# Performance work log

Measured on AMD Instinct MI355X. Metric: run time of the kernel, lower is better.

The kernel has to match this reference:

```python
import jax, jax.numpy as jnp
import numpy as np
from jax import lax

V = 32000   # vocab_size (len(word2id)+1)
I = 512     # txt_input_size (embedding dim / LSTM input)
H = 1024    # txt_hidden_size
IMG = 2048  # img_input_size == img_hidden_size (hidden_fc input)
B = 64      # batch
T = 64      # target length (decode runs T-1 steps)


def setup_inputs() -> dict:
    key = jax.random.key(0)
    ks = jax.random.split(key, 16)
    n = lambda k, shape, s=0.02: jax.random.normal(k, shape, jnp.float32) * s
    embed = n(ks[0], (V, I)).at[0].set(0.0)  # padding_idx=0 row is zero
    return {
        "src": jax.random.normal(ks[1], (B, IMG), jnp.float32),
        "tgt_ids": jax.random.randint(ks[2], (B, T), 0, V),
        "embed": embed,
        "W_h": n(ks[3], (H, IMG)), "b_h": jnp.zeros((H,), jnp.float32),
        "W_c": n(ks[4], (H, IMG)), "b_c": jnp.zeros((H,), jnp.float32),
        "W_ih": n(ks[5], (4 * H, I)), "W_hh": n(ks[6], (4 * H, H)),
        "b_ih": jnp.zeros((4 * H,), jnp.float32),
        "b_hh": jnp.zeros((4 * H,), jnp.float32),
        "W_out": n(ks[7], (V, H)), "b_out": jnp.zeros((V,), jnp.float32),
    }


def reference(src, tgt_ids, embed, W_h, b_h, W_c, b_c,
              W_ih, W_hh, b_ih, b_hh, W_out, b_out):
    # init_hidden: tanh(Linear(src)) for both hidden and cell
    h0 = jnp.tanh(src @ W_h.T + b_h)  # [B, H]
    c0 = jnp.tanh(src @ W_c.T + b_c)  # [B, H]

    x = embed[tgt_ids]                 # [B, T, I]
    xs = jnp.swapaxes(x[:, :-1, :], 0, 1)  # [T-1, B, I] teacher-forced inputs

    def step(carry, xt):
        h, c = carry
        g = xt @ W_ih.T + b_ih + h @ W_hh.T + b_hh  # [B, 4H], gate order i,f,g,o
        i, f, gg, o = jnp.split(g, 4, axis=-1)
        c = jax.nn.sigmoid(f) * c + jax.nn.sigmoid(i) * jnp.tanh(gg)
        h = jax.nn.sigmoid(o) * jnp.tanh(c)
        return (h, c), h

    _, hs = lax.scan(step, (h0, c0), xs)        # [T-1, B, H]
    outs = jnp.swapaxes(hs, 0, 1)               # [B, T-1, H]
    # dropout is identity in eval / deterministic reference
    logits = jnp.einsum('bth,vh->btv', outs, W_out) + b_out  # [B, T-1, V]
    logp = jax.nn.log_softmax(logits, axis=-1)

    tgt = tgt_ids[:, 1:]                        # [B, T-1]
    tok_lp = jnp.take_along_axis(logp, tgt[..., None], axis=2)[..., 0]
    mask = (tgt != 0)
    num_words = mask.sum()
    loss = -(tok_lp * mask).sum() / jnp.maximum(num_words, 1).astype(jnp.float32)
    return loss, num_words
```

## Files before the change

kernel.cpp:

```cpp
#include <hip/hip_runtime.h>
#include <math.h>

static constexpr int BB = 64;
static constexpr int TT = 64;
static constexpr int VV = 32000;
static constexpr int II = 512;
static constexpr int HH = 1024;
static constexpr int GG = 2048;
static constexpr int NT = 63;
static constexpr int NR = NT * BB;
static constexpr int MP = 4096;
static constexpr int NVB = 500;
static constexpr int VBS = 512;

using s16x8 = __attribute__((ext_vector_type(8))) short;
using f32x4 = __attribute__((ext_vector_type(4))) float;

__device__ __forceinline__ unsigned short f2bf(float f) {
    union { float f; unsigned u; } v; v.f = f;
    unsigned r = v.u + 0x7FFFu + ((v.u >> 16) & 1u);
    return (unsigned short)(r >> 16);
}
__device__ __forceinline__ float bf2f(unsigned short h) {
    union { unsigned u; float f; } v; v.u = ((unsigned)h) << 16;
    return v.f;
}

__device__ __forceinline__ void gload_lds16(const unsigned short* g,
                                            unsigned short* l) {
    __builtin_amdgcn_global_load_lds(
        (const __attribute__((address_space(1))) void*)g,
        (__attribute__((address_space(3))) void*)l, 16, 0, 0);
}

__global__ void cvt_kernel(const float* __restrict__ in,
                           unsigned short* __restrict__ out, int n4) {
    int idx = blockIdx.x * blockDim.x + threadIdx.x;
    int stride = gridDim.x * blockDim.x;
    for (int i = idx; i < n4; i += stride) {
        float4 v = ((const float4*)in)[i];
        ushort4 o;
        o.x = f2bf(v.x); o.y = f2bf(v.y); o.z = f2bf(v.z); o.w = f2bf(v.w);
        ((ushort4*)out)[i] = o;
    }
}

__global__ void gather_kernel(const float* __restrict__ embed,
                              const int* __restrict__ tgt_ids,
                              unsigned short* __restrict__ X,
                              int* __restrict__ TGT) {
    int idx = blockIdx.x * 256 + threadIdx.x;
    if (idx >= NR * (II / 4)) return;
    int r = idx / (II / 4);
    int kq = idx % (II / 4);
    int t = r / BB, b = r % BB;
    int tok = tgt_ids[b * TT + t];
    float4 v = ((const float4*)(embed + (size_t)tok * II))[kq];
    ushort4 o;
    o.x = f2bf(v.x); o.y = f2bf(v.y); o.z = f2bf(v.z); o.w = f2bf(v.w);
    ((ushort4*)(X + (size_t)r * II))[kq] = o;
    if (kq == 0) TGT[r] = tgt_ids[b * TT + t + 1];
}

__global__ __launch_bounds__(256) void init_hc_kernel(
    const float* __restrict__ src,
    const float* __restrict__ W_h, const float* __restrict__ b_h,
    const float* __restrict__ W_c, const float* __restrict__ b_c,
    unsigned short* __restrict__ HS, float* __restrict__ C) {
    int wave = blockIdx.x * 4 + (threadIdx.x >> 6);
    int lane = threadIdx.x & 63;
    int sel = wave >> 13;
    int rem = wave & 8191;
    int j = rem >> 3;
    int b0 = (rem & 7) * 8;
    const float* w = (sel ? W_c : W_h) + (size_t)j * GG;
    float acc[8] = {0.f,0.f,0.f,0.f,0.f,0.f,0.f,0.f};
    for (int k = lane; k < GG; k += 64) {
        float wv = w[k];
#pragma unroll
        for (int bb = 0; bb < 8; ++bb)
            acc[bb] += wv * src[(size_t)(b0 + bb) * GG + k];
    }
#pragma unroll
    for (int bb = 0; bb < 8; ++bb)
        for (int off = 32; off; off >>= 1)
            acc[bb] += __shfl_xor(acc[bb], off);
    if (lane == 0) {
        float bias = sel ? b_c[j] : b_h[j];
#pragma unroll
        for (int bb = 0; bb < 8; ++bb) {
            float v = tanhf(acc[bb] + bias);
            if (sel == 0) HS[(size_t)(b0 + bb) * HH + j] = f2bf(v);
            else          C[(size_t)(b0 + bb) * HH + j] = v;
        }
    }
}

template<int KTOT>
__device__ __forceinline__ void gemm_body(
    const unsigned short* __restrict__ Abase,
    const unsigned short* __restrict__ Bbase,
    unsigned short* Al, unsigned short* Bl,
    int tid, f32x4 (&acc)[4][4]) {
    int wv = tid >> 6, lane = tid & 63;
    int rl = lane & 15, lg = lane >> 4;
    int wr = wv >> 1, wc = wv & 1;
    int sw = rl & 7;
    for (int kc = 0; kc < KTOT; kc += 64) {
        if (kc) __syncthreads();
#pragma unroll
        for (int it = 0; it < 4; ++it) {
            int c = it * 256 + tid;
            int row = c >> 3, slot = c & 7;
            int sslot = slot ^ (row & 7);
            gload_lds16(Abase + (size_t)row * KTOT + kc + sslot * 8,
                        Al + (size_t)c * 8);
            gload_lds16(Bbase + (size_t)row * KTOT + kc + sslot * 8,
                        Bl + (size_t)c * 8);
        }
        __syncthreads();
#pragma unroll
        for (int ks = 0; ks < 2; ++ks) {
            int soff = ((ks * 4 + lg) ^ sw) * 8;
            s16x8 a[4], b[4];
#pragma unroll
            for (int mf = 0; mf < 4; ++mf)
                a[mf] = *(const s16x8*)&Al[(wr * 64 + mf * 16 + rl) * 64 + soff];
#pragma unroll
            for (int nf = 0; nf < 4; ++nf)
                b[nf] = *(const s16x8*)&Bl[(wc * 64 + nf * 16 + rl) * 64 + soff];
#pragma unroll
            for (int mf = 0; mf < 4; ++mf)
#pragma unroll
                for (int nf = 0; nf < 4; ++nf)
                    acc[mf][nf] = __builtin_amdgcn_mfma_f32_16x16x32_bf16(
                        a[mf], b[nf], acc[mf][nf], 0, 0, 0);
        }
    }
}

__global__ __launch_bounds__(256) void gx_kernel(
    const unsigned short* __restrict__ X,
    const unsigned short* __restrict__ Wih,
    const float* __restrict__ b_ih, const float* __restrict__ b_hh,
    unsigned short* __restrict__ Gx) {
    __shared__ unsigned short Al[128 * 64];
    __shared__ unsigned short Bl[128 * 64];
    int tid = threadIdx.x;
    int mblk = blockIdx.x, nblk = blockIdx.y;
    int rbase = mblk * 128, v0 = nblk * 128;
    f32x4 acc[4][4];
#pragma unroll
    for (int mf = 0; mf < 4; ++mf)
#pragma unroll
        for (int nf = 0; nf < 4; ++nf) acc[mf][nf] = (f32x4){0.f,0.f,0.f,0.f};
    gemm_body<II>(X + (size_t)rbase * II, Wih + (size_t)v0 * II, Al, Bl, tid, acc);
    int wv = tid >> 6, lane = tid & 63;
    int rl = lane & 15, lg = lane >> 4;
    int wr = wv >> 1, wc = wv & 1;
    float bsum[4];
#pragma unroll
    for (int nf = 0; nf < 4; ++nf) {
        int col = v0 + wc * 64 + nf * 16 + rl;
        bsum[nf] = b_ih[col] + b_hh[col];
    }
#pragma unroll
    for (int mf = 0; mf < 4; ++mf)
#pragma unroll
        for (int q = 0; q < 4; ++q) {
            int r = rbase + wr * 64 + mf * 16 + lg * 4 + q;
#pragma unroll
            for (int nf = 0; nf < 4; ++nf) {
                int col = v0 + wc * 64 + nf * 16 + rl;
                Gx[(size_t)r * 4096 + col] = f2bf(acc[mf][nf][q] + bsum[nf]);
            }
        }
}

__global__ __launch_bounds__(256) void lstm_step_kernel(
    unsigned short* __restrict__ HS,
    const unsigned short* __restrict__ Gx,
    const unsigned short* __restrict__ Whh,
    float* __restrict__ C, int t) {
    __shared__ float R[64 * 16];
    int tid = threadIdx.x;
    int wv = tid >> 6, lane = tid & 63;
    int rl = lane & 15, lg = lane >> 4;
    int u0 = blockIdx.x * 4;
    int grow = tid >> 2, gul = tid & 3;
    int gu = u0 + gul;
    const unsigned short* gx = Gx + (size_t)(t * BB + grow) * 4096 + gu;
    unsigned short gx0 = gx[0 * HH], gx1 = gx[1 * HH];
    unsigned short gx2 = gx[2 * HH], gx3 = gx[3 * HH];
    float cold = C[(size_t)grow * HH + gu];
    const unsigned short* h = HS + (size_t)t * (BB * HH);
    const unsigned short* Ab = h + (size_t)(wv * 16 + rl) * HH + lg * 8;
    int gate = rl >> 2, ul = rl & 3;
    const unsigned short* Bb = Whh + (size_t)(gate * HH + u0 + ul) * HH + lg * 8;
    f32x4 acc0 = {0.f,0.f,0.f,0.f}, acc1 = {0.f,0.f,0.f,0.f};
#pragma unroll
    for (int kc = 0; kc < HH; kc += 64) {
        s16x8 a0 = *(const s16x8*)(Ab + kc);
        s16x8 b0 = *(const s16x8*)(Bb + kc);
        acc0 = __builtin_amdgcn_mfma_f32_16x16x32_bf16(a0, b0, acc0, 0, 0, 0);
        s16x8 a1 = *(const s16x8*)(Ab + kc + 32);
        s16x8 b1 = *(const s16x8*)(Bb + kc + 32);
        acc1 = __builtin_amdgcn_mfma_f32_16x16x32_bf16(a1, b1, acc1, 0, 0, 0);
    }
    f32x4 acc = acc0 + acc1;
#pragma unroll
    for (int q = 0; q < 4; ++q) R[(wv * 16 + lg * 4 + q) * 16 + rl] = acc[q];
    __syncthreads();
    float iv = R[grow * 16 + 0 * 4 + gul] + bf2f(gx0);
    float fv = R[grow * 16 + 1 * 4 + gul] + bf2f(gx1);
    float gv = R[grow * 16 + 2 * 4 + gul] + bf2f(gx2);
    float ov = R[grow * 16 + 3 * 4 + gul] + bf2f(gx3);
    float si = 1.f / (1.f + __expf(-iv));
    float sf = 1.f / (1.f + __expf(-fv));
    float so = 1.f / (1.f + __expf(-ov));
    float cnew = sf * cold + si * tanhf(gv);
    float hv = so * tanhf(cnew);
    C[(size_t)grow * HH + gu] = cnew;
    HS[(size_t)(t + 1) * (BB * HH) + (size_t)grow * HH + gu] = f2bf(hv);
}

__global__ __launch_bounds__(256) void logits_kernel(
    const unsigned short* __restrict__ A,
    const unsigned short* __restrict__ Wo,
    const float* __restrict__ b_out,
    const int* __restrict__ TGT,
    float* __restrict__ PM, float* __restrict__ PS,
    float* __restrict__ TLOG) {
    __shared__ unsigned short Al[128 * 64];
    __shared__ unsigned short Bl[128 * 64];
    int tid = threadIdx.x;
    int mblk = blockIdx.x, nblk = blockIdx.y;
    int rbase = mblk * 128, v0 = nblk * 128;
    f32x4 acc[4][4];
#pragma unroll
    for (int mf = 0; mf < 4; ++mf)
#pragma unroll
        for (int nf = 0; nf < 4; ++nf) acc[mf][nf] = (f32x4){0.f,0.f,0.f,0.f};
    gemm_body<HH>(A + (size_t)rbase * HH, Wo + (size_t)v0 * HH, Al, Bl, tid, acc);
    int wv = tid >> 6, lane = tid & 63;
    int rl = lane & 15, lg = lane >> 4;
    int wr = wv >> 1, wc = wv & 1;
    int cb = v0 + wc * 64;
    float bo[4];
#pragma unroll
    for (int nf = 0; nf < 4; ++nf) bo[nf] = b_out[cb + nf * 16 + rl];
    int vb = nblk * 2 + wc;
#pragma unroll
    for (int mf = 0; mf < 4; ++mf) {
        int rb = rbase + wr * 64 + mf * 16 + lg * 4;
#pragma unroll
        for (int q = 0; q < 4; ++q) {
            int r = rb + q;
            int tg = TGT[r];
            float e[4];
            float m = -1e30f;
#pragma unroll
            for (int nf = 0; nf < 4; ++nf) {
                e[nf] = acc[mf][nf][q] + bo[nf];
                if (cb + nf * 16 + rl == tg) TLOG[r] = e[nf];
                m = fmaxf(m, e[nf]);
            }
#pragma unroll
            for (int msk = 1; msk < 16; msk <<= 1) m = fmaxf(m, __shfl_xor(m, msk));
            float s = 0.f;
#pragma unroll
            for (int nf = 0; nf < 4; ++nf) s += __expf(e[nf] - m);
#pragma unroll
            for (int msk = 1; msk < 16; msk <<= 1) s += __shfl_xor(s, msk);
            if (rl == 0) {
                PM[(size_t)r * VBS + vb] = m;
                PS[(size_t)r * VBS + vb] = s;
            }
        }
    }
}

__global__ void rowred_kernel(const float* __restrict__ PM,
                              const float* __restrict__ PS,
                              const float* __restrict__ TLOG,
                              const int* __restrict__ TGT,
                              float* __restrict__ ROWLP) {
    int r = blockIdx.x * 4 + (threadIdx.x >> 6);
    int lane = threadIdx.x & 63;
    if (r >= NR) return;
    const float* pm = PM + (size_t)r * VBS;
    const float* ps = PS + (size_t)r * VBS;
    float m = -1e30f;
    for (int vb = lane; vb < NVB; vb += 64) m = fmaxf(m, pm[vb]);
    for (int off = 32; off; off >>= 1) m = fmaxf(m, __shfl_xor(m, off));
    float s = 0.f;
    for (int vb = lane; vb < NVB; vb += 64) s += ps[vb] * __expf(pm[vb] - m);
    for (int off = 32; off; off >>= 1) s += __shfl_xor(s, off);
    if (lane == 0) {
        float lse = m + logf(s);
        float lp = TLOG[r] - lse;
        ROWLP[r] = (TGT[r] != 0) ? lp : 0.f;
    }
}

__global__ void final_kernel(const float* __restrict__ ROWLP,
                             const int* __restrict__ TGT,
                             float* __restrict__ out) {
    int tid = threadIdx.x;
    float sum = 0.f; int cnt = 0;
    for (int r = tid; r < NR; r += 256) {
        sum += ROWLP[r];
        cnt += (TGT[r] != 0);
    }
    for (int off = 32; off; off >>= 1) {
        sum += __shfl_xor(sum, off);
        cnt += __shfl_xor(cnt, off);
    }
    __shared__ float wsum[4];
    __shared__ int wcnt[4];
    if ((tid & 63) == 0) { wsum[tid >> 6] = sum; wcnt[tid >> 6] = cnt; }
    __syncthreads();
    if (tid == 0) {
        float S = wsum[0] + wsum[1] + wsum[2] + wsum[3];
        int Cc = wcnt[0] + wcnt[1] + wcnt[2] + wcnt[3];
        out[0] = -S / fmaxf((float)Cc, 1.f);
        out[1] = (float)Cc;
    }
}

extern "C" void kernel_launch(void* const* d_in, const int* in_sizes, int n_in,
                              void* d_out, int out_size, void* d_ws, size_t ws_size,
                              hipStream_t stream) {
    const float* src    = (const float*)d_in[0];
    const int*   tgtids = (const int*)d_in[1];
    const float* embed  = (const float*)d_in[2];
    const float* W_h    = (const float*)d_in[3];
    const float* b_h    = (const float*)d_in[4];
    const float* W_c    = (const float*)d_in[5];
    const float* b_c    = (const float*)d_in[6];
    const float* W_ih   = (const float*)d_in[7];
    const float* W_hh   = (const float*)d_in[8];
    const float* b_ih   = (const float*)d_in[9];
    const float* b_hh   = (const float*)d_in[10];
    const float* W_out  = (const float*)d_in[11];
    const float* b_out  = (const float*)d_in[12];
    float* out = (float*)d_out;

    char* ws = (char*)d_ws;
    size_t off = 0;
    auto alloc = [&](size_t bytes) {
        size_t cur = off;
        off += (bytes + 255) & ~(size_t)255;
        return cur;
    };
    unsigned short* Wo_bf  = (unsigned short*)(ws + alloc((size_t)VV * HH * 2));
    unsigned short* Whh_bf = (unsigned short*)(ws + alloc((size_t)4 * HH * HH * 2));
    unsigned short* Wih_bf = (unsigned short*)(ws + alloc((size_t)4 * HH * II * 2));
    unsigned short* X_bf   = (unsigned short*)(ws + alloc((size_t)MP * II * 2));
    unsigned short* HS     = (unsigned short*)(ws + alloc((size_t)65 * BB * HH * 2));
    float* Cst   = (float*)(ws + alloc((size_t)BB * HH * 4));
    unsigned short* Gx = (unsigned short*)(ws + alloc((size_t)MP * 4096 * 2));
    float* PM    = (float*)(ws + alloc((size_t)MP * VBS * 4));
    float* PS    = (float*)(ws + alloc((size_t)MP * VBS * 4));
    float* TLOG  = (float*)(ws + alloc((size_t)MP * 4));
    int*   TGT   = (int*)(ws + alloc((size_t)MP * 4));
    float* ROWLP = (float*)(ws + alloc((size_t)NR * 4));

    cvt_kernel<<<4096, 256, 0, stream>>>(W_out, Wo_bf, VV * HH / 4);
    cvt_kernel<<<1024, 256, 0, stream>>>(W_hh, Whh_bf, 4 * HH * HH / 4);
    cvt_kernel<<<512, 256, 0, stream>>>(W_ih, Wih_bf, 4 * HH * II / 4);
    gather_kernel<<<(NR * (II / 4) + 255) / 256, 256, 0, stream>>>(embed, tgtids, X_bf, TGT);
    init_hc_kernel<<<4096, 256, 0, stream>>>(src, W_h, b_h, W_c, b_c, HS, Cst);
    gx_kernel<<<dim3(MP / 128, 4096 / 128), 256, 0, stream>>>(
        X_bf, Wih_bf, b_ih, b_hh, Gx);
    for (int t = 0; t < NT; ++t) {
        lstm_step_kernel<<<256, 256, 0, stream>>>(HS, Gx, Whh_bf, Cst, t);
    }
    logits_kernel<<<dim3(MP / 128, VV / 128), 256, 0, stream>>>(
        HS + (size_t)BB * HH, Wo_bf, b_out, TGT, PM, PS, TLOG);
    rowred_kernel<<<NR / 4, 256, 0, stream>>>(PM, PS, TLOG, TGT, ROWLP);
    final_kernel<<<1, 256, 0, stream>>>(ROWLP, TGT, out);
}
```

Before: 1.087 ms.

## Stage W_hh slice in LDS and widen LSTM step blocks to 16 units

Each LSTM step block now handles 16 hidden units with 1024 threads. It first stages the corresponding 64 rows of W_hh into padded shared memory, and 16 waves share the h reads and the staged weights. The goal is to stop re-fetching the hidden state from global memory by many small blocks and to reuse weights across the four M tiles. In exchange, only 64 blocks launch per step, leaving most CUs idle, and each step pays an LDS staging phase plus a barrier.

```diff
diff --git a/kernel.cpp b/kernel.cpp
--- a/kernel.cpp
+++ b/kernel.cpp
@@ -177,26 +177,37 @@
         }
 }
 
-__global__ __launch_bounds__(256) void lstm_step_kernel(
+static constexpr int BSTR = 1032;
+__global__ __launch_bounds__(1024, 1) void lstm_step_kernel(
     unsigned short* __restrict__ HS,
     const unsigned short* __restrict__ Gx,
     const unsigned short* __restrict__ Whh,
     float* __restrict__ C, int t) {
-    __shared__ float R[64 * 16];
+    __shared__ unsigned short Bs[64 * BSTR];
+    __shared__ float R[64 * 68];
     int tid = threadIdx.x;
-    int wv = tid >> 6, lane = tid & 63;
-    int rl = lane & 15, lg = lane >> 4;
-    int u0 = blockIdx.x * 4;
-    int grow = tid >> 2, gul = tid & 3;
+    int u0 = blockIdx.x * 16;
+    int grow = tid >> 4, gul = tid & 15;
     int gu = u0 + gul;
     const unsigned short* gx = Gx + (size_t)(t * BB + grow) * 4096 + gu;
     unsigned short gx0 = gx[0 * HH], gx1 = gx[1 * HH];
     unsigned short gx2 = gx[2 * HH], gx3 = gx[3 * HH];
     float cold = C[(size_t)grow * HH + gu];
-    const unsigned short* h = HS + (size_t)t * (BB * HH);
-    const unsigned short* Ab = h + (size_t)(wv * 16 + rl) * HH + lg * 8;
-    int gate = rl >> 2, ul = rl & 3;
-    const unsigned short* Bb = Whh + (size_t)(gate * HH + u0 + ul) * HH + lg * 8;
+#pragma unroll
+    for (int it = 0; it < 8; ++it) {
+        int id = it * 1024 + tid;
+        int br = id >> 7, k8 = (id & 127) * 8;
+        int ul = br >> 2, g = br & 3;
+        *(uint4*)&Bs[br * BSTR + k8] =
+            *(const uint4*)(Whh + (size_t)(g * HH + u0 + ul) * HH + k8);
+    }
+    __syncthreads();
+    int wv = tid >> 6, lane = tid & 63;
+    int mt = wv >> 2, nt = wv & 3;
+    int rl = lane & 15, lg = lane >> 4;
+    const unsigned short* Ab =
+        HS + (size_t)t * (BB * HH) + (size_t)(mt * 16 + rl) * HH + lg * 8;
+    const unsigned short* Bb = Bs + (nt * 16 + rl) * BSTR + lg * 8;
     f32x4 acc0 = {0.f,0.f,0.f,0.f}, acc1 = {0.f,0.f,0.f,0.f};
 #pragma unroll
     for (int kc = 0; kc < HH; kc += 64) {
@@ -209,16 +220,18 @@
     }
     f32x4 acc = acc0 + acc1;
 #pragma unroll
-    for (int q = 0; q < 4; ++q) R[(wv * 16 + lg * 4 + q) * 16 + rl] = acc[q];
+    for (int q = 0; q < 4; ++q)
+        R[(mt * 16 + lg * 4 + q) * 68 + nt * 16 + rl] = acc[q];
     __syncthreads();
-    float iv = R[grow * 16 + 0 * 4 + gul] + bf2f(gx0);
-    float fv = R[grow * 16 + 1 * 4 + gul] + bf2f(gx1);
-    float gv = R[grow * 16 + 2 * 4 + gul] + bf2f(gx2);
-    float ov = R[grow * 16 + 3 * 4 + gul] + bf2f(gx3);
+    float4 gv4 = *(const float4*)&R[grow * 68 + gul * 4];
+    float iv = gv4.x + bf2f(gx0);
+    float fv = gv4.y + bf2f(gx1);
+    float gg = gv4.z + bf2f(gx2);
+    float ov = gv4.w + bf2f(gx3);
     float si = 1.f / (1.f + __expf(-iv));
     float sf = 1.f / (1.f + __expf(-fv));
     float so = 1.f / (1.f + __expf(-ov));
-    float cnew = sf * cold + si * tanhf(gv);
+    float cnew = sf * cold + si * tanhf(gg);
     float hv = so * tanhf(cnew);
     C[(size_t)grow * HH + gu] = cnew;
     HS[(size_t)(t + 1) * (BB * HH) + (size_t)grow * HH + gu] = f2bf(hv);
@@ -374,7 +387,7 @@
     gx_kernel<<<dim3(MP / 128, 4096 / 128), 256, 0, stream>>>(
         X_bf, Wih_bf, b_ih, b_hh, Gx);
     for (int t = 0; t < NT; ++t) {
-        lstm_step_kernel<<<256, 256, 0, stream>>>(HS, Gx, Whh_bf, Cst, t);
+        lstm_step_kernel<<<64, 1024, 0, stream>>>(HS, Gx, Whh_bf, Cst, t);
     }
     logits_kernel<<<dim3(MP / 128, VV / 128), 256, 0, stream>>>(
         HS + (size_t)BB * HH, Wo_bf, b_out, TGT, PM, PS, TLOG);
```

After: 1.584 ms. +45.8%, slower.
